# Performance work log

Measured on AMD Instinct MI355X. Metric: run time of the kernel, lower is better.

Reference implementation:

```python
import jax, jax.numpy as jnp
import numpy as np

B, NH, T, D = 2, 16, 2048, 64

def setup_inputs() -> dict:
    key = jax.random.key(0)
    kq, kk, kv = jax.random.split(key, 3)
    Q = jax.random.normal(kq, (B, NH, T, D), dtype=jnp.float32)
    K = jax.random.normal(kk, (B, NH, T, D), dtype=jnp.float32)
    V = jax.random.normal(kv, (B, NH, T, D), dtype=jnp.float32)
    return {"Q": Q, "K": K, "V": V}

def reference(Q, K, V):
    # scores: [B, nh, T, T]
    Dh = Q.shape[-1]
    scale = 1.0 / jnp.sqrt(jnp.asarray(Dh, Q.dtype))
    scores = jnp.einsum('bhtd,bhsd->bhts', Q, K) * scale
    Tq = Q.shape[2]
    causal = jnp.tril(jnp.ones((Tq, Tq), dtype=bool))
    scores = jnp.where(causal, scores, jnp.asarray(-jnp.inf, scores.dtype))
    attn = jax.nn.softmax(scores, axis=-1)
    return jnp.einsum('bhts,bhsd->bhtd', attn, V)
```

## Files before the change

kernel.cpp:

```cpp
#include <hip/hip_runtime.h>
#include <hip/hip_bf16.h>


typedef __bf16 bf16;
typedef __bf16 bf16x4 __attribute__((ext_vector_type(4)));
typedef __bf16 bf16x8 __attribute__((ext_vector_type(8)));
typedef float floatx4 __attribute__((ext_vector_type(4)));

#define T_SEQ 2048
#define DH 64
#define TKS 32
#define BHN 32
#define CEXP 0.18033688011112042f

__device__ __forceinline__ void gload16(const bf16* g, bf16* l) {
    __builtin_amdgcn_global_load_lds(
        (const __attribute__((address_space(1))) void*)g,
        (__attribute__((address_space(3))) void*)l, 16, 0, 0);
}

__global__ __launch_bounds__(256) void prep(const float* __restrict__ K,
                                            const float* __restrict__ V,
                                            bf16* __restrict__ Kb,
                                            bf16* __restrict__ Vt) {
    const int bid = (int)blockIdx.x;
    const int tid = (int)threadIdx.x;
    if (bid < 512) {
        size_t i = ((size_t)bid * 256 + tid) * 8;
        #pragma unroll
        for (int it = 0; it < 4; ++it) {
            float4 a = *(const float4*)(K + i + 0);
            float4 b = *(const float4*)(K + i + 4);
            bf16x8 o;
            o[0]=(bf16)(a.x*CEXP); o[1]=(bf16)(a.y*CEXP); o[2]=(bf16)(a.z*CEXP); o[3]=(bf16)(a.w*CEXP);
            o[4]=(bf16)(b.x*CEXP); o[5]=(bf16)(b.y*CEXP); o[6]=(bf16)(b.z*CEXP); o[7]=(bf16)(b.w*CEXP);
            *(bf16x8*)(Kb + i) = o;
            i += (size_t)512 * 256 * 8;
        }
        return;
    }
    __shared__ bf16 tile[2][64][72];
    const int vb = bid - 512;
    const int bh = vb & (BHN - 1);
    const int tp = (vb >> 5) * 128;
    #pragma unroll
    for (int tt = 0; tt < 2; ++tt) {
        const int r = tid >> 2;
        const int c = (tid & 3) * 16;
        const float* s = V + ((size_t)bh * T_SEQ + tp + tt * 64 + r) * DH + c;
        float4 f0 = *(const float4*)(s + 0);
        float4 f1 = *(const float4*)(s + 4);
        float4 f2 = *(const float4*)(s + 8);
        float4 f3 = *(const float4*)(s + 12);
        bf16x8 p0, p1;
        p0[0]=(bf16)f0.x; p0[1]=(bf16)f0.y; p0[2]=(bf16)f0.z; p0[3]=(bf16)f0.w;
        p0[4]=(bf16)f1.x; p0[5]=(bf16)f1.y; p0[6]=(bf16)f1.z; p0[7]=(bf16)f1.w;
        p1[0]=(bf16)f2.x; p1[1]=(bf16)f2.y; p1[2]=(bf16)f2.z; p1[3]=(bf16)f2.w;
        p1[4]=(bf16)f3.x; p1[5]=(bf16)f3.y; p1[6]=(bf16)f3.z; p1[7]=(bf16)f3.w;
        *(bf16x8*)&tile[tt][r][c + 0] = p0;
        *(bf16x8*)&tile[tt][r][c + 8] = p1;
    }
    __syncthreads();
    #pragma unroll
    for (int tt = 0; tt < 2; ++tt) {
        const int d   = tid >> 2;
        const int tch = (tid & 3) * 16;
        bf16x8 o0, o1;
        #pragma unroll
        for (int j = 0; j < 8; ++j) { o0[j] = tile[tt][tch + j][d]; o1[j] = tile[tt][tch + 8 + j][d]; }
        bf16* o = Vt + ((size_t)bh * DH + d) * T_SEQ + tp + tt * 64 + tch;
        *(bf16x8*)(o + 0) = o0;
        *(bf16x8*)(o + 8) = o1;
    }
}

__global__ __launch_bounds__(256, 2)
void fa_fwd(const float* __restrict__ Qg, const bf16* __restrict__ Kb,
            const bf16* __restrict__ Vt, float* __restrict__ Og)
{
    __shared__ __align__(16) bf16 smem[24576];

    const int gid = (int)blockIdx.x;
    const int bh  = gid & (BHN - 1);
    const int m   = gid >> 5;
    const int B   = 64 - 2 * m;
    const int qh  = (31 - m) * 64;
    const int ql  = m * 64;

    const int tid  = (int)threadIdx.x;
    const int wave = tid >> 6;
    const int lane = tid & 63;
    const int quad = lane >> 4;
    const int l16  = lane & 15;
    const int psw  = (l16 >> 1) & 3;

    const int tw0 = (wave < 2) ? wave * 17 : 34 + (wave - 2) * 16;
    const int tw1 = tw0 + ((wave < 2) ? 17 : 16);

    bf16* W = smem + wave * 6144;

    const bf16* Kbh = Kb + (size_t)bh * (T_SEQ * DH);
    const bf16* Vbh = Vt + (size_t)bh * (DH * T_SEQ);
    const size_t qrb = (size_t)bh * T_SEQ;

    const int rl  = lane >> 3;
    const int kch = (lane & 7) ^ (rl & 7);
    const int vr  = lane >> 2;
    const int vch = (lane & 3) ^ ((lane >> 3) & 3);

    bool heavyNow = (tw0 < B);
    int  qbase    = heavyNow ? qh : ql;
    bool hasPark  = false;

    bf16x8 qb[4][2];
    auto loadQ = [&](int qb0) {
        #pragma unroll
        for (int nt = 0; nt < 4; ++nt) {
            const int qrow = qb0 + nt * 16 + l16;
            #pragma unroll
            for (int kk = 0; kk < 2; ++kk) {
                const float* s = Qg + (qrb + qrow) * DH + kk * 32 + quad * 8;
                float4 f0 = *(const float4*)(s);
                float4 f1 = *(const float4*)(s + 4);
                bf16x8 t;
                t[0]=(bf16)f0.x; t[1]=(bf16)f0.y; t[2]=(bf16)f0.z; t[3]=(bf16)f0.w;
                t[4]=(bf16)f1.x; t[5]=(bf16)f1.y; t[6]=(bf16)f1.z; t[7]=(bf16)f1.w;
                qb[nt][kk] = t;
            }
        }
    };
    loadQ(qbase);

    floatx4 oacc[4][4];
    #pragma unroll
    for (int mt = 0; mt < 4; ++mt)
        #pragma unroll
        for (int nt = 0; nt < 4; ++nt) oacc[mt][nt] = (floatx4){0.f,0.f,0.f,0.f};
    float lpart[4] = {0.f, 0.f, 0.f, 0.f};
    bf16x4 parked[16];
    #pragma unroll
    for (int f = 0; f < 16; ++f) parked[f] = (bf16x4){(bf16)0.f,(bf16)0.f,(bf16)0.f,(bf16)0.f};
    float lpark[4] = {0.f, 0.f, 0.f, 0.f};

    auto kTileOf = [&](int t) { return (t < B) ? t : (t - B); };

    auto stageK = [&](int kt, bf16* dst) {
        const bf16* kg = Kbh + (size_t)kt * TKS * DH;
        #pragma unroll
        for (int g = 0; g < 4; ++g)
            gload16(kg + (size_t)(g * 8 + rl) * DH + kch * 8, dst + g * 512);
    };
    auto stageV = [&](int kt, bf16* dst) {
        const bf16* vg = Vbh + kt * TKS;
        #pragma unroll
        for (int g = 0; g < 4; ++g)
            gload16(vg + (size_t)(g * 16 + vr) * T_SEQ + vch * 8, dst + g * 512);
    };

    stageK(kTileOf(tw0), W);
    stageV(kTileOf(tw0), W + 4096);

    for (int t = tw0; t < tw1; ++t) {
        if (heavyNow && t == B) {
            #pragma unroll
            for (int f = 0; f < 16; ++f) {
                bf16x4 w;
                #pragma unroll
                for (int e = 0; e < 4; ++e) w[e] = (bf16)oacc[f >> 2][f & 3][e];
                parked[f] = w;
            }
            #pragma unroll
            for (int nt = 0; nt < 4; ++nt) { lpark[nt] = lpart[nt]; lpart[nt] = 0.f; }
            #pragma unroll
            for (int mt = 0; mt < 4; ++mt)
                #pragma unroll
                for (int nt = 0; nt < 4; ++nt) oacc[mt][nt] = (floatx4){0.f,0.f,0.f,0.f};
            hasPark = true;
            heavyNow = false;
            qbase = ql;
            loadQ(ql);
        }

        const int cur = (t - tw0) & 1;
        bf16* Kcur = W + cur * 2048;
        bf16* Vcur = W + 4096;
        bf16* Pw   = Kcur;
        const int kt = kTileOf(t);
        const int k0 = kt * TKS;

        const bool pf = (t + 1 < tw1);
        if (pf) {
            stageK(kTileOf(t + 1), W + (cur ^ 1) * 2048);
            __builtin_amdgcn_s_waitcnt(0x0F78);
        } else {
            __builtin_amdgcn_s_waitcnt(0x0F70);
        }

        floatx4 sa[2][4];
        #pragma unroll
        for (int mt = 0; mt < 2; ++mt)
            #pragma unroll
            for (int nt = 0; nt < 4; ++nt) sa[mt][nt] = (floatx4){0.f,0.f,0.f,0.f};
        __builtin_amdgcn_s_setprio(1);
        #pragma unroll
        for (int kk = 0; kk < 2; ++kk) {
            #pragma unroll
            for (int mt = 0; mt < 2; ++mt) {
                bf16x8 kf = *(const bf16x8*)&Kcur[(mt * 16 + l16) * 64 + (((kk * 4 + quad) ^ (l16 & 7)) * 8)];
                #pragma unroll
                for (int nt = 0; nt < 4; ++nt)
                    sa[mt][nt] = __builtin_amdgcn_mfma_f32_16x16x32_bf16(kf, qb[nt][kk], sa[mt][nt], 0, 0, 0);
            }
        }
        __builtin_amdgcn_s_setprio(0);
        if (k0 + TKS - 1 > qbase) {
            #pragma unroll
            for (int mt = 0; mt < 2; ++mt)
                #pragma unroll
                for (int nt = 0; nt < 4; ++nt) {
                    const int qg = qbase + nt * 16 + l16;
                    #pragma unroll
                    for (int r = 0; r < 4; ++r) {
                        const int keyg = k0 + mt * 16 + quad * 4 + r;
                        if (keyg > qg) sa[mt][nt][r] = -INFINITY;
                    }
                }
        }
        #pragma unroll
        for (int mt = 0; mt < 2; ++mt)
            #pragma unroll
            for (int nt = 0; nt < 4; ++nt) {
                bf16x4 w;
                #pragma unroll
                for (int r = 0; r < 4; ++r) {
                    const float pv = __builtin_amdgcn_exp2f(sa[mt][nt][r]);
                    lpart[nt] += pv;
                    w[r] = (bf16)pv;
                }
                const int slot = (mt * 2 + (quad >> 1)) ^ psw;
                *(bf16x4*)&Pw[(nt * 16 + l16) * 32 + slot * 8 + (quad & 1) * 4] = w;
            }
        bf16x8 pfr[4];
        #pragma unroll
        for (int nt = 0; nt < 4; ++nt)
            pfr[nt] = *(const bf16x8*)&Pw[(nt * 16 + l16) * 32 + ((quad ^ psw) * 8)];
        if (pf) __builtin_amdgcn_s_waitcnt(0x0F74);
        bf16x8 vf[4];
        #pragma unroll
        for (int mt = 0; mt < 4; ++mt)
            vf[mt] = *(const bf16x8*)&Vcur[(mt * 16 + l16) * 32 + ((quad ^ psw) * 8)];
        if (pf) {
            __builtin_amdgcn_s_waitcnt(0xC07F);
            stageV(kTileOf(t + 1), Vcur);
        }
        __builtin_amdgcn_s_setprio(1);
        #pragma unroll
        for (int mt = 0; mt < 4; ++mt) {
            #pragma unroll
            for (int nt = 0; nt < 4; ++nt)
                oacc[mt][nt] = __builtin_amdgcn_mfma_f32_16x16x32_bf16(vf[mt], pfr[nt], oacc[mt][nt], 0, 0, 0);
        }
        __builtin_amdgcn_s_setprio(0);
    }

    __syncthreads();
    const bool hH = (tw0 < B);
    const bool hL = (tw1 > B);
    if (wave >= 1 && hH) {
        bf16* a = smem + (wave - 1) * 4608;
        float* al = (float*)(a + 4096);
        #pragma unroll
        for (int f = 0; f < 16; ++f) {
            bf16x4 w;
            if (hasPark) w = parked[f];
            else {
                #pragma unroll
                for (int e = 0; e < 4; ++e) w[e] = (bf16)oacc[f >> 2][f & 3][e];
            }
            *(bf16x4*)&a[(f * 64 + lane) * 4] = w;
        }
        #pragma unroll
        for (int nt = 0; nt < 4; ++nt)
            al[nt * 64 + lane] = hasPark ? lpark[nt] : lpart[nt];
    }
    if (wave >= 2 && hL) {
        bf16* a = smem + (wave + 1) * 4608;
        float* al = (float*)(a + 4096);
        #pragma unroll
        for (int f = 0; f < 16; ++f) {
            bf16x4 w;
            #pragma unroll
            for (int e = 0; e < 4; ++e) w[e] = (bf16)oacc[f >> 2][f & 3][e];
            *(bf16x4*)&a[(f * 64 + lane) * 4] = w;
        }
        #pragma unroll
        for (int nt = 0; nt < 4; ++nt)
            al[nt * 64 + lane] = lpart[nt];
    }
    __syncthreads();

    if (wave <= 1) {
        int qfin;
        if (wave == 0) {
            qfin = qh;
            const int nA = (B > 50) ? 3 : ((B > 34) ? 2 : 1);
            for (int i = 0; i < nA; ++i) {
                const bf16* a = smem + i * 4608;
                const float* al = (const float*)(a + 4096);
                #pragma unroll
                for (int f = 0; f < 16; ++f) {
                    bf16x4 w = *(const bf16x4*)&a[(f * 64 + lane) * 4];
                    #pragma unroll
                    for (int e = 0; e < 4; ++e) oacc[f >> 2][f & 3][e] += (float)w[e];
                }
                #pragma unroll
                for (int nt = 0; nt < 4; ++nt) lpart[nt] += al[nt * 64 + lane];
            }
        } else {
            qfin = ql;
            #pragma unroll
            for (int mt = 0; mt < 4; ++mt)
                #pragma unroll
                for (int nt = 0; nt < 4; ++nt) oacc[mt][nt] = (floatx4){0.f,0.f,0.f,0.f};
            #pragma unroll
            for (int nt = 0; nt < 4; ++nt) lpart[nt] = 0.f;
            const int i0 = (B < 50) ? 3 : 4;
            for (int i = i0; i <= 4; ++i) {
                const bf16* a = smem + i * 4608;
                const float* al = (const float*)(a + 4096);
                #pragma unroll
                for (int f = 0; f < 16; ++f) {
                    bf16x4 w = *(const bf16x4*)&a[(f * 64 + lane) * 4];
                    #pragma unroll
                    for (int e = 0; e < 4; ++e) oacc[f >> 2][f & 3][e] += (float)w[e];
                }
                #pragma unroll
                for (int nt = 0; nt < 4; ++nt) lpart[nt] += al[nt * 64 + lane];
            }
        }
        float invl[4];
        #pragma unroll
        for (int nt = 0; nt < 4; ++nt) {
            float v = lpart[nt];
            v += __shfl_xor(v, 16);
            v += __shfl_xor(v, 32);
            invl[nt] = 1.0f / v;
        }
        #pragma unroll
        for (int nt = 0; nt < 4; ++nt) {
            const size_t qrow = qrb + qfin + nt * 16 + l16;
            #pragma unroll
            for (int mt = 0; mt < 4; ++mt) {
                float4 o;
                o.x = oacc[mt][nt][0] * invl[nt];
                o.y = oacc[mt][nt][1] * invl[nt];
                o.z = oacc[mt][nt][2] * invl[nt];
                o.w = oacc[mt][nt][3] * invl[nt];
                *(float4*)&Og[qrow * DH + mt * 16 + quad * 4] = o;
            }
        }
    }
}

extern "C" void kernel_launch(void* const* d_in, const int* in_sizes, int n_in,
                              void* d_out, int out_size, void* d_ws, size_t ws_size,
                              hipStream_t stream) {
    const float* Q = (const float*)d_in[0];
    const float* K = (const float*)d_in[1];
    const float* V = (const float*)d_in[2];
    float* O = (float*)d_out;
    (void)in_sizes; (void)n_in; (void)out_size; (void)ws_size;

    const size_t nelem = (size_t)BHN * T_SEQ * DH;
    bf16* Kbf = (bf16*)d_ws;
    bf16* Vtb = Kbf + nelem;

    prep<<<dim3(1024), dim3(256), 0, stream>>>(K, V, Kbf, Vtb);
    fa_fwd<<<dim3(512), dim3(256), 0, stream>>>(Q, Kbf, Vtb, O);
}
```

Measured before the change: 120.7 us.

## Software-pipeline QK^T one tile ahead and spill parked accumulators to scratch

Restructures the per-wave loop so the QK^T MFMA for the next key tile runs while the current tile's softmax and PV are in flight. K is now prefetched two tiles deep, with waitcnt values adjusted to match. The Q reload and the parking of the heavy accumulator move to the boundary after PV. Parked outputs go into an opaque private array (scratch memory) instead of registers, which frees VGPRs but adds scratch traffic and makes the waitcnt ordering more fragile.

```diff
diff --git a/kernel.cpp b/kernel.cpp
--- a/kernel.cpp
+++ b/kernel.cpp
@@ -108,6 +108,10 @@
     const int vr  = lane >> 2;
     const int vch = (lane & 3) ^ ((lane >> 3) & 3);
 
+    uint pbuf[36];
+    uint* pp = pbuf;
+    asm volatile("" : "+v"(pp));
+
     bool heavyNow = (tw0 < B);
     int  qbase    = heavyNow ? qh : ql;
     bool hasPark  = false;
@@ -137,10 +141,6 @@
         #pragma unroll
         for (int nt = 0; nt < 4; ++nt) oacc[mt][nt] = (floatx4){0.f,0.f,0.f,0.f};
     float lpart[4] = {0.f, 0.f, 0.f, 0.f};
-    bf16x4 parked[16];
-    #pragma unroll
-    for (int f = 0; f < 16; ++f) parked[f] = (bf16x4){(bf16)0.f,(bf16)0.f,(bf16)0.f,(bf16)0.f};
-    float lpark[4] = {0.f, 0.f, 0.f, 0.f};
 
     auto kTileOf = [&](int t) { return (t < B) ? t : (t - B); };
 
@@ -157,62 +157,38 @@
             gload16(vg + (size_t)(g * 16 + vr) * T_SEQ + vch * 8, dst + g * 512);
     };
 
+    const floatx4 zf4 = {0.f, 0.f, 0.f, 0.f};
+    floatx4 sa[2][4];
+    auto computeS = [&](const bf16* Kbuf) {
+        #pragma unroll
+        for (int kk = 0; kk < 2; ++kk)
+            #pragma unroll
+            for (int mt = 0; mt < 2; ++mt) {
+                bf16x8 kf = *(const bf16x8*)&Kbuf[(mt * 16 + l16) * 64 + (((kk * 4 + quad) ^ (l16 & 7)) * 8)];
+                #pragma unroll
+                for (int nt = 0; nt < 4; ++nt)
+                    sa[mt][nt] = __builtin_amdgcn_mfma_f32_16x16x32_bf16(
+                        kf, qb[nt][kk], (kk == 0) ? zf4 : sa[mt][nt], 0, 0, 0);
+            }
+    };
+
     stageK(kTileOf(tw0), W);
+    stageK(kTileOf(tw0 + 1), W + 2048);
     stageV(kTileOf(tw0), W + 4096);
+    __builtin_amdgcn_s_waitcnt(0x0F78);
+    computeS(W);
+    int cur = 0;
 
     for (int t = tw0; t < tw1; ++t) {
-        if (heavyNow && t == B) {
-            #pragma unroll
-            for (int f = 0; f < 16; ++f) {
-                bf16x4 w;
-                #pragma unroll
-                for (int e = 0; e < 4; ++e) w[e] = (bf16)oacc[f >> 2][f & 3][e];
-                parked[f] = w;
-            }
-            #pragma unroll
-            for (int nt = 0; nt < 4; ++nt) { lpark[nt] = lpart[nt]; lpart[nt] = 0.f; }
-            #pragma unroll
-            for (int mt = 0; mt < 4; ++mt)
-                #pragma unroll
-                for (int nt = 0; nt < 4; ++nt) oacc[mt][nt] = (floatx4){0.f,0.f,0.f,0.f};
-            hasPark = true;
-            heavyNow = false;
-            qbase = ql;
-            loadQ(ql);
-        }
-
-        const int cur = (t - tw0) & 1;
+        const bool hasD = (t + 1 < tw1);
+        const bool hasC = (t + 2 < tw1);
+        if (heavyNow && t + 1 == B) loadQ(ql);
+
         bf16* Kcur = W + cur * 2048;
-        bf16* Vcur = W + 4096;
-        bf16* Pw   = Kcur;
-        const int kt = kTileOf(t);
-        const int k0 = kt * TKS;
-
-        const bool pf = (t + 1 < tw1);
-        if (pf) {
-            stageK(kTileOf(t + 1), W + (cur ^ 1) * 2048);
-            __builtin_amdgcn_s_waitcnt(0x0F78);
-        } else {
-            __builtin_amdgcn_s_waitcnt(0x0F70);
-        }
-
-        floatx4 sa[2][4];
-        #pragma unroll
-        for (int mt = 0; mt < 2; ++mt)
-            #pragma unroll
-            for (int nt = 0; nt < 4; ++nt) sa[mt][nt] = (floatx4){0.f,0.f,0.f,0.f};
-        __builtin_amdgcn_s_setprio(1);
-        #pragma unroll
-        for (int kk = 0; kk < 2; ++kk) {
-            #pragma unroll
-            for (int mt = 0; mt < 2; ++mt) {
-                bf16x8 kf = *(const bf16x8*)&Kcur[(mt * 16 + l16) * 64 + (((kk * 4 + quad) ^ (l16 & 7)) * 8)];
-                #pragma unroll
-                for (int nt = 0; nt < 4; ++nt)
-                    sa[mt][nt] = __builtin_amdgcn_mfma_f32_16x16x32_bf16(kf, qb[nt][kk], sa[mt][nt], 0, 0, 0);
-            }
-        }
-        __builtin_amdgcn_s_setprio(0);
+        bf16* Knxt = W + (cur ^ 1) * 2048;
+        bf16* Vb   = W + 4096;
+        const int k0 = kTileOf(t) * TKS;
+
         if (k0 + TKS - 1 > qbase) {
             #pragma unroll
             for (int mt = 0; mt < 2; ++mt)
@@ -238,20 +214,30 @@
                     w[r] = (bf16)pv;
                 }
                 const int slot = (mt * 2 + (quad >> 1)) ^ psw;
-                *(bf16x4*)&Pw[(nt * 16 + l16) * 32 + slot * 8 + (quad & 1) * 4] = w;
+                *(bf16x4*)&Kcur[(nt * 16 + l16) * 32 + slot * 8 + (quad & 1) * 4] = w;
             }
         bf16x8 pfr[4];
         #pragma unroll
         for (int nt = 0; nt < 4; ++nt)
-            pfr[nt] = *(const bf16x8*)&Pw[(nt * 16 + l16) * 32 + ((quad ^ psw) * 8)];
-        if (pf) __builtin_amdgcn_s_waitcnt(0x0F74);
+            pfr[nt] = *(const bf16x8*)&Kcur[(nt * 16 + l16) * 32 + ((quad ^ psw) * 8)];
+        __builtin_amdgcn_s_waitcnt(0xC07F);
+        if (hasC) stageK(kTileOf(t + 2), Kcur);
+        if (hasD) {
+            if (hasC) __builtin_amdgcn_s_waitcnt(0x0F78);
+            else      __builtin_amdgcn_s_waitcnt(0x0F74);
+            __builtin_amdgcn_s_setprio(1);
+            computeS(Knxt);
+            __builtin_amdgcn_s_setprio(0);
+        }
+        if (hasC) __builtin_amdgcn_s_waitcnt(0x0F74);
+        else      __builtin_amdgcn_s_waitcnt(0x0F70);
         bf16x8 vf[4];
         #pragma unroll
         for (int mt = 0; mt < 4; ++mt)
-            vf[mt] = *(const bf16x8*)&Vcur[(mt * 16 + l16) * 32 + ((quad ^ psw) * 8)];
-        if (pf) {
+            vf[mt] = *(const bf16x8*)&Vb[(mt * 16 + l16) * 32 + ((quad ^ psw) * 8)];
+        if (hasD) {
             __builtin_amdgcn_s_waitcnt(0xC07F);
-            stageV(kTileOf(t + 1), Vcur);
+            stageV(kTileOf(t + 1), Vb);
         }
         __builtin_amdgcn_s_setprio(1);
         #pragma unroll
@@ -261,6 +247,29 @@
                 oacc[mt][nt] = __builtin_amdgcn_mfma_f32_16x16x32_bf16(vf[mt], pfr[nt], oacc[mt][nt], 0, 0, 0);
         }
         __builtin_amdgcn_s_setprio(0);
+        if (heavyNow && t + 1 == B) {
+            #pragma unroll
+            for (int f = 0; f < 16; ++f) {
+                bf16x4 w;
+                #pragma unroll
+                for (int e = 0; e < 4; ++e) w[e] = (bf16)oacc[f >> 2][f & 3][e];
+                uint2 u; __builtin_memcpy(&u, &w, 8);
+                pp[f * 2] = u.x; pp[f * 2 + 1] = u.y;
+            }
+            #pragma unroll
+            for (int nt = 0; nt < 4; ++nt) {
+                pp[32 + nt] = __float_as_uint(lpart[nt]);
+                lpart[nt] = 0.f;
+            }
+            #pragma unroll
+            for (int mt = 0; mt < 4; ++mt)
+                #pragma unroll
+                for (int nt = 0; nt < 4; ++nt) oacc[mt][nt] = (floatx4){0.f,0.f,0.f,0.f};
+            hasPark = true;
+            heavyNow = false;
+            qbase = ql;
+        }
+        cur ^= 1;
     }
 
     __syncthreads();
@@ -272,8 +281,10 @@
         #pragma unroll
         for (int f = 0; f < 16; ++f) {
             bf16x4 w;
-            if (hasPark) w = parked[f];
-            else {
+            if (hasPark) {
+                uint2 u; u.x = pp[f * 2]; u.y = pp[f * 2 + 1];
+                __builtin_memcpy(&w, &u, 8);
+            } else {
                 #pragma unroll
                 for (int e = 0; e < 4; ++e) w[e] = (bf16)oacc[f >> 2][f & 3][e];
             }
@@ -281,7 +292,7 @@
         }
         #pragma unroll
         for (int nt = 0; nt < 4; ++nt)
-            al[nt * 64 + lane] = hasPark ? lpark[nt] : lpart[nt];
+            al[nt * 64 + lane] = hasPark ? __uint_as_float(pp[32 + nt]) : lpart[nt];
     }
     if (wave >= 2 && hL) {
         bf16* a = smem + (wave + 1) * 4608;
```

New measurement: 129.6 us. +7.4%, slower.
